# Optimization experiments

Hardware: AMD Instinct MI355X
Metric: run time of the kernel (lower is better)

## Reference

```python
import jax, jax.numpy as jnp
import numpy as np

N_NODES = 256
N_SECRETS = 64
N_INPUTS = 16      # per-node source-node inputs
N_SECDEP = 8       # per-node secret-dependency columns
ENTRIES = 3 + N_INPUTS + N_SECDEP  # 27
ACTION_SIZE = 4096
BATCH = 8192
STATE_DIM = N_NODES + N_SECRETS + 2  # 322


def _build_index_matrix() -> np.ndarray:
    """idx[i] = column indices of `state` concatenated for node i, mirroring split()."""
    rng = np.random.default_rng(1234)
    idx = np.empty((N_NODES, ENTRIES), dtype=np.int32)
    g0 = N_NODES + N_SECRETS  # first of the two global columns
    for i in range(N_NODES):
        src = rng.integers(0, N_NODES, size=N_INPUTS)           # inputs[j].sourceNodeIndex
        sec = N_NODES + rng.choice(N_SECRETS, size=N_SECDEP, replace=False)  # secrIndex[i]
        idx[i] = np.concatenate(([i, g0, g0 + 1], src, np.sort(sec)))
    return idx


def setup_inputs() -> dict:
    key = jax.random.key(0)
    k1, k2, k3, k4 = jax.random.split(key, 4)
    state = jax.random.normal(k1, (BATCH, STATE_DIM), dtype=jnp.float32)
    # per-node Linear(ENTRIES, 1): weight [N, E], bias [N]
    bound = 1.0 / np.sqrt(ENTRIES)
    W = jax.random.uniform(k2, (N_NODES, ENTRIES), jnp.float32, -bound, bound)
    b = jax.random.uniform(k3, (N_NODES,), jnp.float32, -bound, bound)
    # final Linear(N_NODES, ACTION_SIZE, bias=False): weight [A, N]
    bf = 1.0 / np.sqrt(N_NODES)
    Wf = jax.random.uniform(k4, (ACTION_SIZE, N_NODES), jnp.float32, -bf, bf)
    idx = jnp.asarray(_build_index_matrix())
    return {"state": state, "W": W, "b": b, "Wf": Wf, "idx": idx}


def reference(state, W, b, Wf, idx):
    # split(): per-node gather of ENTRIES columns -> [B, N, E]
    gathered = jnp.take(state, idx, axis=1)
    # per-node tiny Linear + tanh -> [B, N]
    y = jnp.tanh(jnp.einsum("bne,ne->bn", gathered, W) + b)
    # final linear (no bias), scaled sigmoid -> [B, A]
    return 500.0 * jax.nn.sigmoid(jnp.einsum("bn,an->ba", y, Wf))
```

## Files before the change

### kernel.cpp

```cpp
#include <hip/hip_runtime.h>
#include <cmath>

#define ENTRIES 27
#define ACTION  4096
#define BATCH   8192
#define SDIM    322
#define KPAD    352
#define NNODES  256

typedef unsigned short u16;
typedef u16 u16x4 __attribute__((ext_vector_type(4)));
typedef u16 u16x8 __attribute__((ext_vector_type(8)));
typedef __bf16 bf16x8 __attribute__((ext_vector_type(8)));
typedef float floatx2 __attribute__((ext_vector_type(2)));
typedef float floatx4 __attribute__((ext_vector_type(4)));

__device__ __forceinline__ u16 f2bf(float f) {
    unsigned u = __builtin_bit_cast(unsigned, f);
    unsigned r = (u + 0x7FFFu + ((u >> 16) & 1u)) >> 16;
    return (u16)r;
}
__device__ __forceinline__ float sig500(float v) {
    return __fdividef(500.0f, 1.0f + __expf(-v));
}
__device__ __forceinline__ float ftanh(float x) {
    return 1.0f - __fdividef(2.0f, __expf(2.0f * x) + 1.0f);
}
__device__ __forceinline__ void gl_lds16(const u16* g, u16* l) {
    __builtin_amdgcn_global_load_lds(
        (const __attribute__((address_space(1))) unsigned int*)g,
        (__attribute__((address_space(3))) unsigned int*)l, 16, 0, 0);
}

#define PREP_WF0 32
#define PREP_TOT 1056

__global__ __launch_bounds__(256) void prep_kernel(
    const float* __restrict__ W, const int* __restrict__ idx,
    const float* __restrict__ wf,
    u16* __restrict__ wg, u16* __restrict__ wfb)
{
    const int tid = threadIdx.x;
    const int bid = blockIdx.x;

    if (bid < PREP_WF0) {
        __shared__ float rows[8 * KPAD];
        for (int i = tid; i < 8 * KPAD; i += 256) rows[i] = 0.f;
        __syncthreads();
        if (tid < 8 * ENTRIES) {
            const int nl = tid / ENTRIES;
            const int e  = tid - nl * ENTRIES;
            const int n  = bid * 8 + nl;
            atomicAdd(&rows[nl * KPAD + idx[n * ENTRIES + e]],
                      W[n * ENTRIES + e]);
        }
        __syncthreads();
        for (int i = tid; i < 8 * KPAD; i += 256)
            wg[(size_t)bid * 8 * KPAD + i] = f2bf(rows[i]);
    } else {
        const int i0 = ((bid - PREP_WF0) * 256 + tid) * 4;
        floatx4 v = *(const floatx4*)(wf + i0);
        u16x4 r;
        r.x = f2bf(v.x); r.y = f2bf(v.y); r.z = f2bf(v.z); r.w = f2bf(v.w);
        *(u16x4*)(wfb + i0) = r;
    }
}

__global__ __launch_bounds__(256) void gemm1_fused(
    const float* __restrict__ state, const u16* __restrict__ wg,
    u16* __restrict__ y, const float* __restrict__ bias)
{
    __shared__ u16 Bs[64 * KPAD];
    __shared__ u16 As[64 * 32];

    const int bm   = blockIdx.x;
    const int bn   = blockIdx.y;
    const int tid  = threadIdx.x;
    const int lane = tid & 63;
    const int wave = tid >> 6;
    const int wm   = wave & 1;
    const int wn   = wave >> 1;
    const int l15  = lane & 15;
    const int koff = (lane >> 4) << 3;

    const u16* wgp = wg + (size_t)bn * 64 * KPAD;
    for (int c = wave; c < 44; c += 4)
        gl_lds16(wgp + c * 512 + lane * 8, &Bs[c * 512]);

    const int arow = tid >> 2;
    const int qseg = tid & 3;
    const float* ap = state + (size_t)(bm * 64 + arow) * SDIM + qseg * 8;
    float va[8];

    auto loada = [&](int kk) {
        const int c0 = kk + qseg * 8;
        const float* p = ap + kk;
        if (c0 + 8 <= SDIM) {
#pragma unroll
            for (int j = 0; j < 4; j++)
                *(floatx2*)&va[2 * j] = *(const floatx2*)(p + 2 * j);
        } else {
#pragma unroll
            for (int j = 0; j < 8; j++)
                va[j] = (c0 + j < SDIM) ? p[j] : 0.f;
        }
    };
    loada(0);

    floatx4 acc[2][2];
#pragma unroll
    for (int mi = 0; mi < 2; mi++)
#pragma unroll
        for (int ni = 0; ni < 2; ni++)
            acc[mi][ni] = (floatx4){0.f, 0.f, 0.f, 0.f};

#pragma unroll
    for (int s = 0; s < 11; s++) {
        const int kk = s * 32;
        u16x8 pk;
#pragma unroll
        for (int j = 0; j < 8; j++) ((u16*)&pk)[j] = f2bf(va[j]);

        __syncthreads();
        *(u16x8*)&As[arow * 32 + qseg * 8] = pk;
        __syncthreads();

        if (s < 10) loada(kk + 32);

        bf16x8 af[2], bfr[2];
#pragma unroll
        for (int mi = 0; mi < 2; mi++)
            af[mi] = __builtin_bit_cast(bf16x8,
                *(const u16x8*)&As[((wm << 5) + (mi << 4) + l15) * 32 + koff]);
#pragma unroll
        for (int ni = 0; ni < 2; ni++)
            bfr[ni] = __builtin_bit_cast(bf16x8,
                *(const u16x8*)&Bs[(wn * 32 + ni * 16 + l15) * KPAD + kk + koff]);
#pragma unroll
        for (int mi = 0; mi < 2; mi++)
#pragma unroll
            for (int ni = 0; ni < 2; ni++)
                acc[mi][ni] = __builtin_amdgcn_mfma_f32_16x16x32_bf16(
                    af[mi], bfr[ni], acc[mi][ni], 0, 0, 0);
    }

    const int r0 = (lane >> 4) << 2;
    float bv[2];
#pragma unroll
    for (int ni = 0; ni < 2; ni++)
        bv[ni] = bias[bn * 64 + wn * 32 + ni * 16 + l15];
#pragma unroll
    for (int mi = 0; mi < 2; mi++)
#pragma unroll
        for (int ni = 0; ni < 2; ni++) {
            const int row = bm * 64 + wm * 32 + mi * 16 + r0;
            const int col = bn * 64 + wn * 32 + ni * 16 + l15;
#pragma unroll
            for (int r = 0; r < 4; r++)
                y[(size_t)(row + r) * NNODES + col] =
                    f2bf(ftanh(acc[mi][ni][r] + bv[ni]));
        }
}

template<int KDIM, int EPI, int BN>
__global__ __launch_bounds__(256) void gemm_mfma(
    const u16* __restrict__ A, const u16* __restrict__ B,
    void* __restrict__ outp, const float* __restrict__ bias)
{
    constexpr int NI  = BN / 32;
    constexpr int WN  = BN / 2;
    constexpr int ACH = 8;
    constexpr int BCH = BN / 16;

    __shared__ u16 As[128 * 32];
    __shared__ u16 Bs[BN * 32];

    const int bm   = blockIdx.x;
    const int bn   = blockIdx.y;
    const int tid  = threadIdx.x;
    const int lane = tid & 63;
    const int wave = tid >> 6;
    const int wm   = wave & 1;
    const int wn   = wave >> 1;
    const int l15  = lane & 15;
    const int koff = (lane >> 4) << 3;

    floatx4 acc[4][NI];
#pragma unroll
    for (int mi = 0; mi < 4; mi++)
#pragma unroll
        for (int ni = 0; ni < NI; ni++)
            acc[mi][ni] = (floatx4){0.f, 0.f, 0.f, 0.f};

    const int crow = lane >> 2;
    const int ckel = (lane & 3) << 3;

#pragma unroll
    for (int kk = 0; kk < KDIM; kk += 32) {
        __syncthreads();
#pragma unroll
        for (int c = wave; c < ACH + BCH; c += 4) {
            const bool isA = c < ACH;
            const int  cr  = isA ? c : c - ACH;
            const int  row = cr * 16 + crow;
            const u16* g = isA
                ? (A + ((size_t)bm * 128 + row) * KDIM + kk + ckel)
                : (B + ((size_t)bn * BN  + row) * KDIM + kk + ckel);
            u16* l = isA ? &As[cr * 512] : &Bs[cr * 512];
            gl_lds16(g, l);
        }
        __syncthreads();

        bf16x8 af[4], bfg[NI];
#pragma unroll
        for (int mi = 0; mi < 4; mi++)
            af[mi] = __builtin_bit_cast(bf16x8,
                *(const u16x8*)&As[((wm << 6) + (mi << 4) + l15) * 32 + koff]);
#pragma unroll
        for (int ni = 0; ni < NI; ni++)
            bfg[ni] = __builtin_bit_cast(bf16x8,
                *(const u16x8*)&Bs[(wn * WN + (ni << 4) + l15) * 32 + koff]);

#pragma unroll
        for (int mi = 0; mi < 4; mi++)
#pragma unroll
            for (int ni = 0; ni < NI; ni++)
                acc[mi][ni] = __builtin_amdgcn_mfma_f32_16x16x32_bf16(
                    af[mi], bfg[ni], acc[mi][ni], 0, 0, 0);
    }

    const int r0 = (lane >> 4) << 2;
    float bv[NI];
    if (EPI == 1) {
#pragma unroll
        for (int ni = 0; ni < NI; ni++)
            bv[ni] = bias[bn * BN + wn * WN + ni * 16 + l15];
    }
#pragma unroll
    for (int mi = 0; mi < 4; mi++) {
#pragma unroll
        for (int ni = 0; ni < NI; ni++) {
            const int row = bm * 128 + wm * 64 + mi * 16 + r0;
            const int col = bn * BN + wn * WN + ni * 16 + l15;
#pragma unroll
            for (int r = 0; r < 4; r++) {
                float v = acc[mi][ni][r];
                if (EPI == 0) {
                    ((float*)outp)[(size_t)(row + r) * ACTION + col] = sig500(v);
                } else {
                    ((u16*)outp)[(size_t)(row + r) * NNODES + col] =
                        f2bf(ftanh(v + bv[ni]));
                }
            }
        }
    }
}

extern "C" void kernel_launch(void* const* d_in, const int* in_sizes, int n_in,
                              void* d_out, int out_size, void* d_ws, size_t ws_size,
                              hipStream_t stream) {
    const float* state = (const float*)d_in[0];
    const float* W     = (const float*)d_in[1];
    const float* b     = (const float*)d_in[2];
    const float* Wf    = (const float*)d_in[3];
    const int*   idx   = (const int*)  d_in[4];
    float* out = (float*)d_out;

    u16* wg  = (u16*)d_ws;
    u16* y   = wg + (size_t)NNODES * KPAD;
    u16* wfb = y  + (size_t)BATCH * NNODES;

    prep_kernel<<<PREP_TOT, 256, 0, stream>>>(W, idx, Wf, wg, wfb);
    gemm1_fused<<<dim3(128, 4), 256, 0, stream>>>(state, wg, y, b);
    gemm_mfma<256, 0, 128><<<dim3(BATCH / 128, ACTION / 128), 256, 0, stream>>>(
        y, wfb, (void*)out, nullptr);
}
```

Baseline: 176.6 us.

## Fold weight prep into first GEMM kernel, dropping a launch

```diff
diff --git a/kernel.cpp b/kernel.cpp
--- a/kernel.cpp
+++ b/kernel.cpp
@@ -5,7 +5,7 @@
 #define ACTION  4096
 #define BATCH   8192
 #define SDIM    322
-#define KPAD    352
+#define KPAD    360
 #define NNODES  256
 
 typedef unsigned short u16;
@@ -32,46 +32,134 @@
         (__attribute__((address_space(3))) unsigned int*)l, 16, 0, 0);
 }
 
-#define PREP_WF0 32
-#define PREP_TOT 1056
-
-__global__ __launch_bounds__(256) void prep_kernel(
-    const float* __restrict__ W, const int* __restrict__ idx,
-    const float* __restrict__ wf,
-    u16* __restrict__ wg, u16* __restrict__ wfb)
+__global__ __launch_bounds__(256) void gemm1_all(
+    const float* __restrict__ state, const float* __restrict__ W,
+    const float* __restrict__ bias,  const float* __restrict__ Wf,
+    const int*   __restrict__ idx,
+    u16* __restrict__ wfb, u16* __restrict__ y)
 {
-    const int tid = threadIdx.x;
-    const int bid = blockIdx.x;
-
-    if (bid < PREP_WF0) {
-        __shared__ float rows[8 * KPAD];
-        for (int i = tid; i < 8 * KPAD; i += 256) rows[i] = 0.f;
+    __shared__ u16 lds[28800];
+    u16*   Bs      = lds;
+    u16*   As      = lds + 64 * KPAD;
+    float* scratch = (float*)(lds + 64 * KPAD);
+
+    const int tid  = threadIdx.x;
+    const int bid  = blockIdx.x;
+    const int lane = tid & 63;
+    const int wave = tid >> 6;
+    const int wm   = wave & 1;
+    const int wn   = wave >> 1;
+    const int l15  = lane & 15;
+    const int koff = (lane >> 4) << 3;
+    const int bm   = bid & 127;
+    const int bn   = bid >> 7;
+
+    {
+        const int i0 = (bid * 256 + tid) * 8;
+        floatx4 v0 = *(const floatx4*)(Wf + i0);
+        floatx4 v1 = *(const floatx4*)(Wf + i0 + 4);
+        u16x8 r;
+        r[0] = f2bf(v0.x); r[1] = f2bf(v0.y); r[2] = f2bf(v0.z); r[3] = f2bf(v0.w);
+        r[4] = f2bf(v1.x); r[5] = f2bf(v1.y); r[6] = f2bf(v1.z); r[7] = f2bf(v1.w);
+        *(u16x8*)(wfb + i0) = r;
+    }
+
+    for (int g = 0; g < 8; g++) {
+        for (int i = tid; i < 8 * KPAD; i += 256) scratch[i] = 0.f;
         __syncthreads();
         if (tid < 8 * ENTRIES) {
             const int nl = tid / ENTRIES;
             const int e  = tid - nl * ENTRIES;
-            const int n  = bid * 8 + nl;
-            atomicAdd(&rows[nl * KPAD + idx[n * ENTRIES + e]],
+            const int n  = bn * 64 + g * 8 + nl;
+            atomicAdd(&scratch[nl * KPAD + idx[n * ENTRIES + e]],
                       W[n * ENTRIES + e]);
         }
         __syncthreads();
         for (int i = tid; i < 8 * KPAD; i += 256)
-            wg[(size_t)bid * 8 * KPAD + i] = f2bf(rows[i]);
-    } else {
-        const int i0 = ((bid - PREP_WF0) * 256 + tid) * 4;
-        floatx4 v = *(const floatx4*)(wf + i0);
-        u16x4 r;
-        r.x = f2bf(v.x); r.y = f2bf(v.y); r.z = f2bf(v.z); r.w = f2bf(v.w);
-        *(u16x4*)(wfb + i0) = r;
-    }
-}
-
-__global__ __launch_bounds__(256) void gemm1_fused(
-    const float* __restrict__ state, const u16* __restrict__ wg,
-    u16* __restrict__ y, const float* __restrict__ bias)
+            Bs[g * 8 * KPAD + i] = f2bf(scratch[i]);
+        __syncthreads();
+    }
+
+    const int arow = tid >> 2;
+    const int qseg = tid & 3;
+    const float* ap = state + (size_t)(bm * 64 + arow) * SDIM + qseg * 8;
+    float va[8];
+    auto loada = [&](int kk) {
+        const int c0 = kk + qseg * 8;
+        const float* p = ap + kk;
+        if (c0 + 8 <= SDIM) {
+#pragma unroll
+            for (int j = 0; j < 4; j++)
+                *(floatx2*)&va[2 * j] = *(const floatx2*)(p + 2 * j);
+        } else {
+#pragma unroll
+            for (int j = 0; j < 8; j++)
+                va[j] = (c0 + j < SDIM) ? p[j] : 0.f;
+        }
+    };
+    loada(0);
+
+    floatx4 acc[2][2];
+#pragma unroll
+    for (int mi = 0; mi < 2; mi++)
+#pragma unroll
+        for (int ni = 0; ni < 2; ni++)
+            acc[mi][ni] = (floatx4){0.f, 0.f, 0.f, 0.f};
+
+#pragma unroll
+    for (int s = 0; s < 11; s++) {
+        const int kk = s * 32;
+        u16x8 pk;
+#pragma unroll
+        for (int j = 0; j < 8; j++) ((u16*)&pk)[j] = f2bf(va[j]);
+
+        __syncthreads();
+        *(u16x8*)&As[arow * 32 + qseg * 8] = pk;
+        __syncthreads();
+
+        if (s < 10) loada(kk + 32);
+
+        bf16x8 af[2], bfr[2];
+#pragma unroll
+        for (int mi = 0; mi < 2; mi++)
+            af[mi] = __builtin_bit_cast(bf16x8,
+                *(const u16x8*)&As[((wm << 5) + (mi << 4) + l15) * 32 + koff]);
+#pragma unroll
+        for (int ni = 0; ni < 2; ni++)
+            bfr[ni] = __builtin_bit_cast(bf16x8,
+                *(const u16x8*)&Bs[(wn * 32 + ni * 16 + l15) * KPAD + kk + koff]);
+#pragma unroll
+        for (int mi = 0; mi < 2; mi++)
+#pragma unroll
+            for (int ni = 0; ni < 2; ni++)
+                acc[mi][ni] = __builtin_amdgcn_mfma_f32_16x16x32_bf16(
+                    af[mi], bfr[ni], acc[mi][ni], 0, 0, 0);
+    }
+
+    const int r0 = (lane >> 4) << 2;
+    float bv[2];
+#pragma unroll
+    for (int ni = 0; ni < 2; ni++)
+        bv[ni] = bias[bn * 64 + wn * 32 + ni * 16 + l15];
+#pragma unroll
+    for (int mi = 0; mi < 2; mi++)
+#pragma unroll
+        for (int ni = 0; ni < 2; ni++) {
+            const int row = bm * 64 + wm * 32 + mi * 16 + r0;
+            const int col = bn * 64 + wn * 32 + ni * 16 + l15;
+#pragma unroll
+            for (int r = 0; r < 4; r++)
+                y[(size_t)(row + r) * NNODES + col] =
+                    f2bf(ftanh(acc[mi][ni][r] + bv[ni]));
+        }
+}
+
+__global__ __launch_bounds__(256) void gemm2(
+    const u16* __restrict__ A, const u16* __restrict__ B,
+    float* __restrict__ out)
 {
-    __shared__ u16 Bs[64 * KPAD];
-    __shared__ u16 As[64 * 32];
+    __shared__ u16 As[128 * 32];
+    __shared__ u16 Bs[128 * 32];
 
     const int bm   = blockIdx.x;
     const int bn   = blockIdx.y;
@@ -83,177 +171,60 @@
     const int l15  = lane & 15;
     const int koff = (lane >> 4) << 3;
 
-    const u16* wgp = wg + (size_t)bn * 64 * KPAD;
-    for (int c = wave; c < 44; c += 4)
-        gl_lds16(wgp + c * 512 + lane * 8, &Bs[c * 512]);
-
-    const int arow = tid >> 2;
-    const int qseg = tid & 3;
-    const float* ap = state + (size_t)(bm * 64 + arow) * SDIM + qseg * 8;
-    float va[8];
-
-    auto loada = [&](int kk) {
-        const int c0 = kk + qseg * 8;
-        const float* p = ap + kk;
-        if (c0 + 8 <= SDIM) {
-#pragma unroll
-            for (int j = 0; j < 4; j++)
-                *(floatx2*)&va[2 * j] = *(const floatx2*)(p + 2 * j);
-        } else {
-#pragma unroll
-            for (int j = 0; j < 8; j++)
-                va[j] = (c0 + j < SDIM) ? p[j] : 0.f;
-        }
-    };
-    loada(0);
-
-    floatx4 acc[2][2];
-#pragma unroll
-    for (int mi = 0; mi < 2; mi++)
-#pragma unroll
-        for (int ni = 0; ni < 2; ni++)
-            acc[mi][ni] = (floatx4){0.f, 0.f, 0.f, 0.f};
-
-#pragma unroll
-    for (int s = 0; s < 11; s++) {
-        const int kk = s * 32;
-        u16x8 pk;
-#pragma unroll
-        for (int j = 0; j < 8; j++) ((u16*)&pk)[j] = f2bf(va[j]);
-
-        __syncthreads();
-        *(u16x8*)&As[arow * 32 + qseg * 8] = pk;
-        __syncthreads();
-
-        if (s < 10) loada(kk + 32);
-
-        bf16x8 af[2], bfr[2];
-#pragma unroll
-        for (int mi = 0; mi < 2; mi++)
-            af[mi] = __builtin_bit_cast(bf16x8,
-                *(const u16x8*)&As[((wm << 5) + (mi << 4) + l15) * 32 + koff]);
-#pragma unroll
-        for (int ni = 0; ni < 2; ni++)
-            bfr[ni] = __builtin_bit_cast(bf16x8,
-                *(const u16x8*)&Bs[(wn * 32 + ni * 16 + l15) * KPAD + kk + koff]);
-#pragma unroll
-        for (int mi = 0; mi < 2; mi++)
-#pragma unroll
-            for (int ni = 0; ni < 2; ni++)
-                acc[mi][ni] = __builtin_amdgcn_mfma_f32_16x16x32_bf16(
-                    af[mi], bfr[ni], acc[mi][ni], 0, 0, 0);
-    }
-
-    const int r0 = (lane >> 4) << 2;
-    float bv[2];
-#pragma unroll
-    for (int ni = 0; ni < 2; ni++)
-        bv[ni] = bias[bn * 64 + wn * 32 + ni * 16 + l15];
-#pragma unroll
-    for (int mi = 0; mi < 2; mi++)
-#pragma unroll
-        for (int ni = 0; ni < 2; ni++) {
-            const int row = bm * 64 + wm * 32 + mi * 16 + r0;
-            const int col = bn * 64 + wn * 32 + ni * 16 + l15;
-#pragma unroll
-            for (int r = 0; r < 4; r++)
-                y[(size_t)(row + r) * NNODES + col] =
-                    f2bf(ftanh(acc[mi][ni][r] + bv[ni]));
-        }
-}
-
-template<int KDIM, int EPI, int BN>
-__global__ __launch_bounds__(256) void gemm_mfma(
-    const u16* __restrict__ A, const u16* __restrict__ B,
-    void* __restrict__ outp, const float* __restrict__ bias)
-{
-    constexpr int NI  = BN / 32;
-    constexpr int WN  = BN / 2;
-    constexpr int ACH = 8;
-    constexpr int BCH = BN / 16;
-
-    __shared__ u16 As[128 * 32];
-    __shared__ u16 Bs[BN * 32];
-
-    const int bm   = blockIdx.x;
-    const int bn   = blockIdx.y;
-    const int tid  = threadIdx.x;
-    const int lane = tid & 63;
-    const int wave = tid >> 6;
-    const int wm   = wave & 1;
-    const int wn   = wave >> 1;
-    const int l15  = lane & 15;
-    const int koff = (lane >> 4) << 3;
-
-    floatx4 acc[4][NI];
+    floatx4 acc[4][4];
 #pragma unroll
     for (int mi = 0; mi < 4; mi++)
 #pragma unroll
-        for (int ni = 0; ni < NI; ni++)
+        for (int ni = 0; ni < 4; ni++)
             acc[mi][ni] = (floatx4){0.f, 0.f, 0.f, 0.f};
 
     const int crow = lane >> 2;
     const int ckel = (lane & 3) << 3;
 
 #pragma unroll
-    for (int kk = 0; kk < KDIM; kk += 32) {
-        __syncthreads();
-#pragma unroll
-        for (int c = wave; c < ACH + BCH; c += 4) {
-            const bool isA = c < ACH;
-            const int  cr  = isA ? c : c - ACH;
+    for (int kk = 0; kk < 256; kk += 32) {
+        __syncthreads();
+#pragma unroll
+        for (int c = wave; c < 16; c += 4) {
+            const bool isA = c < 8;
+            const int  cr  = isA ? c : c - 8;
             const int  row = cr * 16 + crow;
             const u16* g = isA
-                ? (A + ((size_t)bm * 128 + row) * KDIM + kk + ckel)
-                : (B + ((size_t)bn * BN  + row) * KDIM + kk + ckel);
-            u16* l = isA ? &As[cr * 512] : &Bs[cr * 512];
-            gl_lds16(g, l);
-        }
-        __syncthreads();
-
-        bf16x8 af[4], bfg[NI];
+                ? (A + ((size_t)bm * 128 + row) * 256 + kk + ckel)
+                : (B + ((size_t)bn * 128 + row) * 256 + kk + ckel);
+            gl_lds16(g, isA ? &As[cr * 512] : &Bs[cr * 512]);
+        }
+        __syncthreads();
+
+        bf16x8 af[4], bfg[4];
 #pragma unroll
         for (int mi = 0; mi < 4; mi++)
             af[mi] = __builtin_bit_cast(bf16x8,
                 *(const u16x8*)&As[((wm << 6) + (mi << 4) + l15) * 32 + koff]);
 #pragma unroll
-        for (int ni = 0; ni < NI; ni++)
+        for (int ni = 0; ni < 4; ni++)
             bfg[ni] = __builtin_bit_cast(bf16x8,
-                *(const u16x8*)&Bs[(wn * WN + (ni << 4) + l15) * 32 + koff]);
+                *(const u16x8*)&Bs[(wn * 64 + (ni << 4) + l15) * 32 + koff]);
 
 #pragma unroll
         for (int mi = 0; mi < 4; mi++)
 #pragma unroll
-            for (int ni = 0; ni < NI; ni++)
+            for (int ni = 0; ni < 4; ni++)
                 acc[mi][ni] = __builtin_amdgcn_mfma_f32_16x16x32_bf16(
                     af[mi], bfg[ni], acc[mi][ni], 0, 0, 0);
     }
 
     const int r0 = (lane >> 4) << 2;
-    float bv[NI];
-    if (EPI == 1) {
-#pragma unroll
-        for (int ni = 0; ni < NI; ni++)
-            bv[ni] = bias[bn * BN + wn * WN + ni * 16 + l15];
-    }
-#pragma unroll
-    for (int mi = 0; mi < 4; mi++) {
-#pragma unroll
-        for (int ni = 0; ni < NI; ni++) {
+#pragma unroll
+    for (int mi = 0; mi < 4; mi++)
+#pragma unroll
+        for (int ni = 0; ni < 4; ni++) {
             const int row = bm * 128 + wm * 64 + mi * 16 + r0;
-            const int col = bn * BN + wn * WN + ni * 16 + l15;
-#pragma unroll
-            for (int r = 0; r < 4; r++) {
-                float v = acc[mi][ni][r];
-                if (EPI == 0) {
-                    ((float*)outp)[(size_t)(row + r) * ACTION + col] = sig500(v);
-                } else {
-                    ((u16*)outp)[(size_t)(row + r) * NNODES + col] =
-                        f2bf(ftanh(v + bv[ni]));
-                }
-            }
-        }
-    }
+            const int col = bn * 128 + wn * 64 + ni * 16 + l15;
+#pragma unroll
+            for (int r = 0; r < 4; r++)
+                out[(size_t)(row + r) * ACTION + col] = sig500(acc[mi][ni][r]);
+        }
 }
 
 extern "C" void kernel_launch(void* const* d_in, const int* in_sizes, int n_in,
@@ -266,12 +237,9 @@
     const int*   idx   = (const int*)  d_in[4];
     float* out = (float*)d_out;
 
-    u16* wg  = (u16*)d_ws;
-    u16* y   = wg + (size_t)NNODES * KPAD;
-    u16* wfb = y  + (size_t)BATCH * NNODES;
-
-    prep_kernel<<<PREP_TOT, 256, 0, stream>>>(W, idx, Wf, wg, wfb);
-    gemm1_fused<<<dim3(128, 4), 256, 0, stream>>>(state, wg, y, b);
-    gemm_mfma<256, 0, 128><<<dim3(BATCH / 128, ACTION / 128), 256, 0, stream>>>(
-        y, wfb, (void*)out, nullptr);
-}
+    u16* wfb = (u16*)d_ws;
+    u16* y   = wfb + (size_t)ACTION * NNODES;
+
+    gemm1_all<<<512, 256, 0, stream>>>(state, W, b, Wf, idx, wfb, y);
+    gemm2<<<dim3(BATCH / 128, ACTION / 128), 256, 0, stream>>>(y, wfb, out);
+}
```

Measured after the change: 182.3 us. +3.2%, slower.

## Double-buffer second GEMM, remap blocks per XCD, use nontemporal output stores

Applied to the files above, without the earlier changes.

```diff
diff --git a/kernel.cpp b/kernel.cpp
--- a/kernel.cpp
+++ b/kernel.cpp
@@ -5,7 +5,7 @@
 #define ACTION  4096
 #define BATCH   8192
 #define SDIM    322
-#define KPAD    352
+#define KPAD    360
 #define NNODES  256
 
 typedef unsigned short u16;
@@ -84,14 +84,13 @@
     const int koff = (lane >> 4) << 3;
 
     const u16* wgp = wg + (size_t)bn * 64 * KPAD;
-    for (int c = wave; c < 44; c += 4)
+    for (int c = wave; c < 45; c += 4)
         gl_lds16(wgp + c * 512 + lane * 8, &Bs[c * 512]);
 
     const int arow = tid >> 2;
     const int qseg = tid & 3;
     const float* ap = state + (size_t)(bm * 64 + arow) * SDIM + qseg * 8;
     float va[8];
-
     auto loada = [&](int kk) {
         const int c0 = kk + qseg * 8;
         const float* p = ap + kk;
@@ -162,21 +161,18 @@
         }
 }
 
-template<int KDIM, int EPI, int BN>
-__global__ __launch_bounds__(256) void gemm_mfma(
+__global__ __launch_bounds__(256) void gemm2(
     const u16* __restrict__ A, const u16* __restrict__ B,
-    void* __restrict__ outp, const float* __restrict__ bias)
+    float* __restrict__ out)
 {
-    constexpr int NI  = BN / 32;
-    constexpr int WN  = BN / 2;
-    constexpr int ACH = 8;
-    constexpr int BCH = BN / 16;
-
-    __shared__ u16 As[128 * 32];
-    __shared__ u16 Bs[BN * 32];
-
-    const int bm   = blockIdx.x;
-    const int bn   = blockIdx.y;
+    __shared__ u16 As[2][128 * 32];
+    __shared__ u16 Bs[2][128 * 32];
+
+    const int gid  = blockIdx.x;
+    const int xcd  = gid & 7;
+    const int li   = gid >> 3;
+    const int bn   = (xcd << 2) | (li & 3);
+    const int bm   = li >> 2;
     const int tid  = threadIdx.x;
     const int lane = tid & 63;
     const int wave = tid >> 6;
@@ -184,76 +180,69 @@
     const int wn   = wave >> 1;
     const int l15  = lane & 15;
     const int koff = (lane >> 4) << 3;
-
-    floatx4 acc[4][NI];
-#pragma unroll
-    for (int mi = 0; mi < 4; mi++)
-#pragma unroll
-        for (int ni = 0; ni < NI; ni++)
-            acc[mi][ni] = (floatx4){0.f, 0.f, 0.f, 0.f};
-
     const int crow = lane >> 2;
     const int ckel = (lane & 3) << 3;
 
-#pragma unroll
-    for (int kk = 0; kk < KDIM; kk += 32) {
-        __syncthreads();
-#pragma unroll
-        for (int c = wave; c < ACH + BCH; c += 4) {
-            const bool isA = c < ACH;
-            const int  cr  = isA ? c : c - ACH;
+    auto stage = [&](int buf, int kk) {
+#pragma unroll
+        for (int c = wave; c < 16; c += 4) {
+            const bool isA = c < 8;
+            const int  cr  = isA ? c : c - 8;
             const int  row = cr * 16 + crow;
             const u16* g = isA
-                ? (A + ((size_t)bm * 128 + row) * KDIM + kk + ckel)
-                : (B + ((size_t)bn * BN  + row) * KDIM + kk + ckel);
-            u16* l = isA ? &As[cr * 512] : &Bs[cr * 512];
-            gl_lds16(g, l);
-        }
-        __syncthreads();
-
-        bf16x8 af[4], bfg[NI];
+                ? (A + ((size_t)bm * 128 + row) * 256 + kk + ckel)
+                : (B + ((size_t)bn * 128 + row) * 256 + kk + ckel);
+            gl_lds16(g, isA ? &As[buf][cr * 512] : &Bs[buf][cr * 512]);
+        }
+    };
+
+    floatx4 acc[4][4];
+#pragma unroll
+    for (int mi = 0; mi < 4; mi++)
+#pragma unroll
+        for (int ni = 0; ni < 4; ni++)
+            acc[mi][ni] = (floatx4){0.f, 0.f, 0.f, 0.f};
+
+    stage(0, 0);
+    __syncthreads();
+
+#pragma unroll
+    for (int s = 0; s < 8; s++) {
+        const int cur = s & 1;
+        if (s < 7) stage(cur ^ 1, (s + 1) * 32);
+
+        bf16x8 af[4], bfg[4];
 #pragma unroll
         for (int mi = 0; mi < 4; mi++)
             af[mi] = __builtin_bit_cast(bf16x8,
-                *(const u16x8*)&As[((wm << 6) + (mi << 4) + l15) * 32 + koff]);
-#pragma unroll
-        for (int ni = 0; ni < NI; ni++)
+                *(const u16x8*)&As[cur][((wm << 6) + (mi << 4) + l15) * 32 + koff]);
+#pragma unroll
+        for (int ni = 0; ni < 4; ni++)
             bfg[ni] = __builtin_bit_cast(bf16x8,
-                *(const u16x8*)&Bs[(wn * WN + (ni << 4) + l15) * 32 + koff]);
+                *(const u16x8*)&Bs[cur][(wn * 64 + (ni << 4) + l15) * 32 + koff]);
 
 #pragma unroll
         for (int mi = 0; mi < 4; mi++)
 #pragma unroll
-            for (int ni = 0; ni < NI; ni++)
+            for (int ni = 0; ni < 4; ni++)
                 acc[mi][ni] = __builtin_amdgcn_mfma_f32_16x16x32_bf16(
                     af[mi], bfg[ni], acc[mi][ni], 0, 0, 0);
+
+        __syncthreads();
     }
 
     const int r0 = (lane >> 4) << 2;
-    float bv[NI];
-    if (EPI == 1) {
-#pragma unroll
-        for (int ni = 0; ni < NI; ni++)
-            bv[ni] = bias[bn * BN + wn * WN + ni * 16 + l15];
-    }
-#pragma unroll
-    for (int mi = 0; mi < 4; mi++) {
-#pragma unroll
-        for (int ni = 0; ni < NI; ni++) {
+#pragma unroll
+    for (int mi = 0; mi < 4; mi++)
+#pragma unroll
+        for (int ni = 0; ni < 4; ni++) {
             const int row = bm * 128 + wm * 64 + mi * 16 + r0;
-            const int col = bn * BN + wn * WN + ni * 16 + l15;
-#pragma unroll
-            for (int r = 0; r < 4; r++) {
-                float v = acc[mi][ni][r];
-                if (EPI == 0) {
-                    ((float*)outp)[(size_t)(row + r) * ACTION + col] = sig500(v);
-                } else {
-                    ((u16*)outp)[(size_t)(row + r) * NNODES + col] =
-                        f2bf(ftanh(v + bv[ni]));
-                }
-            }
-        }
-    }
+            const int col = bn * 128 + wn * 64 + ni * 16 + l15;
+#pragma unroll
+            for (int r = 0; r < 4; r++)
+                __builtin_nontemporal_store(sig500(acc[mi][ni][r]),
+                    &out[(size_t)(row + r) * ACTION + col]);
+        }
 }
 
 extern "C" void kernel_launch(void* const* d_in, const int* in_sizes, int n_in,
@@ -272,6 +261,5 @@
 
     prep_kernel<<<PREP_TOT, 256, 0, stream>>>(W, idx, Wf, wg, wfb);
     gemm1_fused<<<dim3(128, 4), 256, 0, stream>>>(state, wg, y, b);
-    gemm_mfma<256, 0, 128><<<dim3(BATCH / 128, ACTION / 128), 256, 0, stream>>>(
-        y, wfb, (void*)out, nullptr);
-}
+    gemm2<<<2048, 256, 0, stream>>>(y, wfb, out);
+}
```

After: 189.3 us. +7.2%, slower.
